# Performance work log

Hardware: AMD Instinct MI355X
Metric: run time of the kernel (lower is better)

The kernel has to match this reference:

```python
import jax, jax.numpy as jnp
import numpy as np

N_NODES = 10000
N_EDGES = 80000
LATENT = 128
OUT_SIZE = 3
NODE_F = 12
EDGE_F = 7
STEPS = 15
LN_EPS = 1e-5


def _mlp(x, W0, b0, W1, b1, W2, b2):
    h = jax.nn.relu(x @ W0 + b0)
    h = jax.nn.relu(h @ W1 + b1)
    return h @ W2 + b2


def _ln(x, g, b):
    m = jnp.mean(x, axis=-1, keepdims=True)
    v = jnp.mean(jnp.square(x - m), axis=-1, keepdims=True)
    return (x - m) * jax.lax.rsqrt(v + LN_EPS) * g + b


def _forward(node_features, edge_features, senders, receivers,
             enW0, enb0, enW1, enb1, enW2, enb2, eng, enbe,
             eeW0, eeb0, eeW1, eeb1, eeW2, eeb2, eeg, eebe,
             beW0, beb0, beW1, beb1, beW2, beb2, beg, bebe,
             bnW0, bnb0, bnW1, bnb1, bnW2, bnb2, bng, bnbe,
             dW0, db0, dW1, db1, dW2, db2):
    # Encoder: node and mesh-edge MLPs with LayerNorm
    nl = _ln(_mlp(node_features, enW0, enb0, enW1, enb1, enW2, enb2), eng, enbe)  # [N, L]
    el = _ln(_mlp(edge_features, eeW0, eeb0, eeW1, eeb1, eeW2, eeb2), eeg, eebe)  # [E, L]

    # Processor: 15 GraphNetBlocks with residual connections, scanned over stacked params
    def block(carry, p):
        n, e = carry
        (eW0, eb0, eW1, eb1, eW2, eb2, eg, ebe,
         nW0, nb0, nW1, nb1, nW2, nb2, ng, nbe) = p
        feat = jnp.concatenate([n[senders], n[receivers], e], axis=-1)  # [E, 3L]
        new_e = _ln(_mlp(feat, eW0, eb0, eW1, eb1, eW2, eb2), eg, ebe)  # [E, L]
        agg = jax.ops.segment_sum(new_e, receivers, num_segments=N_NODES)  # [N, L]
        new_n = _ln(_mlp(jnp.concatenate([n, agg], axis=-1), nW0, nb0, nW1, nb1, nW2, nb2), ng, nbe)
        return (n + new_n, e + new_e), None

    xs = (beW0, beb0, beW1, beb1, beW2, beb2, beg, bebe,
          bnW0, bnb0, bnW1, bnb1, bnW2, bnb2, bng, bnbe)
    (nl, el), _ = jax.lax.scan(jax.checkpoint(block), (nl, el), xs)

    # Decoder: MLP without LayerNorm
    return _mlp(nl, dW0, db0, dW1, db1, dW2, db2)  # [N, OUT_SIZE]


def setup_inputs() -> dict:
    ks = iter(jax.random.split(jax.random.key(0), 32))

    def W(*shape):
        return jax.random.normal(next(ks), shape, jnp.float32) * (1.0 / np.sqrt(shape[-2]))

    z = lambda *s: jnp.zeros(s, jnp.float32)
    o = lambda *s: jnp.ones(s, jnp.float32)
    d = {}
    d['node_features'] = jax.random.normal(next(ks), (N_NODES, NODE_F), jnp.float32)
    d['edge_features'] = jax.random.normal(next(ks), (N_EDGES, EDGE_F), jnp.float32)
    d['senders'] = jax.random.randint(next(ks), (N_EDGES,), 0, N_NODES, jnp.int32)
    d['receivers'] = jax.random.randint(next(ks), (N_EDGES,), 0, N_NODES, jnp.int32)
    d.update(enW0=W(NODE_F, LATENT), enb0=z(LATENT), enW1=W(LATENT, LATENT), enb1=z(LATENT),
             enW2=W(LATENT, LATENT), enb2=z(LATENT), eng=o(LATENT), enbe=z(LATENT))
    d.update(eeW0=W(EDGE_F, LATENT), eeb0=z(LATENT), eeW1=W(LATENT, LATENT), eeb1=z(LATENT),
             eeW2=W(LATENT, LATENT), eeb2=z(LATENT), eeg=o(LATENT), eebe=z(LATENT))
    d.update(beW0=W(STEPS, 3 * LATENT, LATENT), beb0=z(STEPS, LATENT),
             beW1=W(STEPS, LATENT, LATENT), beb1=z(STEPS, LATENT),
             beW2=W(STEPS, LATENT, LATENT), beb2=z(STEPS, LATENT),
             beg=o(STEPS, LATENT), bebe=z(STEPS, LATENT))
    d.update(bnW0=W(STEPS, 2 * LATENT, LATENT), bnb0=z(STEPS, LATENT),
             bnW1=W(STEPS, LATENT, LATENT), bnb1=z(STEPS, LATENT),
             bnW2=W(STEPS, LATENT, LATENT), bnb2=z(STEPS, LATENT),
             bng=o(STEPS, LATENT), bnbe=z(STEPS, LATENT))
    d.update(dW0=W(LATENT, LATENT), db0=z(LATENT), dW1=W(LATENT, LATENT), db1=z(LATENT),
             dW2=W(LATENT, OUT_SIZE), db2=z(OUT_SIZE))
    return d


def reference(node_features, edge_features, senders, receivers,
              enW0, enb0, enW1, enb1, enW2, enb2, eng, enbe,
              eeW0, eeb0, eeW1, eeb1, eeW2, eeb2, eeg, eebe,
              beW0, beb0, beW1, beb1, beW2, beb2, beg, bebe,
              bnW0, bnb0, bnW1, bnb1, bnW2, bnb2, bng, bnbe,
              dW0, db0, dW1, db1, dW2, db2):
    return _forward(node_features, edge_features, senders, receivers,
                    enW0, enb0, enW1, enb1, enW2, enb2, eng, enbe,
                    eeW0, eeb0, eeW1, eeb1, eeW2, eeb2, eeg, eebe,
                    beW0, beb0, beW1, beb1, beW2, beb2, beg, bebe,
                    bnW0, bnb0, bnW1, bnb1, bnW2, bnb2, bng, bnbe,
                    dW0, db0, dW1, db1, dW2, db2)
```

## Files before the change

### kernel.cpp

```cpp
#include <hip/hip_runtime.h>
#include <hip/hip_bf16.h>
#include <stdint.h>

#define N_NODES 10000
#define N_EDGES 80000
#define L 128
#define STEPS 15
#define LN_EPS 1e-5f
#define NTHR 256
#define H_STRIDE 272

typedef short short8 __attribute__((ext_vector_type(8)));
typedef float floatx4 __attribute__((ext_vector_type(4)));

__device__ __forceinline__ float bf2f(const __hip_bfloat16 x) {
    return __bfloat162float(x);
}
__device__ __forceinline__ float ldmix(const void* p, int idx, int isf32) {
    return isf32 ? ((const float*)p)[idx]
                 : bf2f(((const __hip_bfloat16*)p)[idx]);
}

__global__ void detect_dtype(const uint32_t* __restrict__ nf, int* cnt) {
    int c = 0;
    for (int i = blockIdx.x * blockDim.x + threadIdx.x; i < 60000;
         i += gridDim.x * blockDim.x) {
        const uint32_t w = nf[i];
        c += (((w >> 7) & 0xFF) >= 0xC6) + (((w >> 23) & 0xFF) >= 0xC6);
    }
    atomicAdd(cnt, c);
}

#define N_TMATS 14
struct TAll {
    const void* src[N_TMATS];
    long long cum[N_TMATS + 1];
    int K[N_TMATS], N[N_TMATS], Kpad[N_TMATS];
};

__global__ void transpose_all(TAll a, const int* __restrict__ cnt,
                              __hip_bfloat16* __restrict__ pool) {
    const int isf32 = (*cnt > 1000);
    const long long total = a.cum[N_TMATS];
    for (long long i = blockIdx.x * (long long)blockDim.x + threadIdx.x;
         i < total; i += gridDim.x * (long long)blockDim.x) {
        int e = 0;
        #pragma unroll 1
        for (int j = 1; j < N_TMATS; j++) if (i >= a.cum[j]) e = j;
        const long long r = i - a.cum[e];
        const int per = a.N[e] * a.Kpad[e];
        const int m = (int)(r / per);
        const int r2 = (int)(r - (long long)m * per);
        const int nn = r2 / a.Kpad[e];
        const int kk = r2 - nn * a.Kpad[e];
        float v = 0.f;
        if (kk < a.K[e]) v = ldmix(a.src[e], (m * a.K[e] + kk) * a.N[e] + nn, isf32);
        pool[i] = __float2bfloat16(v);
    }
}

__global__ void convert_feats(const void* __restrict__ nf,
                              const void* __restrict__ ef,
                              const int* __restrict__ cnt,
                              const int* __restrict__ elist,
                              __hip_bfloat16* __restrict__ fN,
                              __hip_bfloat16* __restrict__ fE)
{
    const int isf32 = (*cnt > 1000);
    const int totN = N_NODES * 32;
    const int totE = N_EDGES * 32;
    for (int i = blockIdx.x * blockDim.x + threadIdx.x; i < totN + totE;
         i += gridDim.x * blockDim.x) {
        if (i < totN) {
            const int r = i >> 5, c = i & 31;
            fN[i] = __float2bfloat16(c < 12 ? ldmix(nf, r * 12 + c, isf32) : 0.f);
        } else {
            const int j = i - totN;
            const int r = j >> 5, c = j & 31;
            const int e = elist[r];
            fE[j] = __float2bfloat16(c < 7 ? ldmix(ef, e * 7 + c, isf32) : 0.f);
        }
    }
}

__global__ void csr_hist(const int* __restrict__ rcv, int* __restrict__ deg) {
    for (int i = blockIdx.x * blockDim.x + threadIdx.x; i < N_EDGES;
         i += gridDim.x * blockDim.x)
        atomicAdd(&deg[rcv[i]], 1);
}

__global__ void csr_scan(const int* __restrict__ deg, int* __restrict__ rowptr,
                         int* __restrict__ cursor) {
    __shared__ int part[256];
    __shared__ int partx[257];
    const int t = threadIdx.x;
    int s = 0;
    for (int j = 0; j < 40; j++) {
        const int i = t * 40 + j;
        if (i < N_NODES) s += deg[i];
    }
    part[t] = s;
    __syncthreads();
    if (t == 0) {
        int r = 0;
        for (int k = 0; k < 256; k++) { partx[k] = r; r += part[k]; }
        partx[256] = r;
    }
    __syncthreads();
    int run = partx[t];
    for (int j = 0; j < 40; j++) {
        const int i = t * 40 + j;
        if (i < N_NODES) {
            rowptr[i] = run;
            cursor[i] = run;
            run += deg[i];
        }
    }
    if (t == 255) rowptr[N_NODES] = partx[256];
}

__global__ void csr_scatter(const int* __restrict__ rcv, int* __restrict__ cursor,
                            int* __restrict__ elist) {
    for (int i = blockIdx.x * blockDim.x + threadIdx.x; i < N_EDGES;
         i += gridDim.x * blockDim.x) {
        const int p = atomicAdd(&cursor[rcv[i]], 1);
        elist[p] = i;
    }
}

__global__ void sort_meta(const int* __restrict__ snd, const int* __restrict__ rcv,
                          const int* __restrict__ elist,
                          int* __restrict__ ssnd, int* __restrict__ srcv) {
    for (int i = blockIdx.x * blockDim.x + threadIdx.x; i < N_EDGES;
         i += gridDim.x * blockDim.x) {
        const int e = elist[i];
        ssnd[i] = snd[e];
        srcv[i] = rcv[e];
    }
}

__global__ __launch_bounds__(256)
void csr_agg(const int* __restrict__ rowptr,
             const __hip_bfloat16* __restrict__ ln16,
             __hip_bfloat16* __restrict__ agg16)
{
    const int g = threadIdx.x >> 5;
    const int lane = threadIdx.x & 31;
    const int v = blockIdx.x * 8 + g;
    if (v >= N_NODES) return;
    const int c0 = lane * 4;
    float s0 = 0.f, s1 = 0.f, s2 = 0.f, s3 = 0.f;
    int j = rowptr[v];
    const int en = rowptr[v + 1];
    for (; j + 1 < en; j += 2) {
        union { uint2 w; __hip_bfloat16 h[4]; } u0, u1;
        u0.w = *(const uint2*)(ln16 + (size_t)j * L + c0);
        u1.w = *(const uint2*)(ln16 + (size_t)(j + 1) * L + c0);
        s0 += bf2f(u0.h[0]); s1 += bf2f(u0.h[1]); s2 += bf2f(u0.h[2]); s3 += bf2f(u0.h[3]);
        s0 += bf2f(u1.h[0]); s1 += bf2f(u1.h[1]); s2 += bf2f(u1.h[2]); s3 += bf2f(u1.h[3]);
    }
    for (; j < en; j++) {
        union { uint2 w; __hip_bfloat16 h[4]; } u;
        u.w = *(const uint2*)(ln16 + (size_t)j * L + c0);
        s0 += bf2f(u.h[0]); s1 += bf2f(u.h[1]); s2 += bf2f(u.h[2]); s3 += bf2f(u.h[3]);
    }
    union { uint2 w; __hip_bfloat16 h[4]; } o;
    o.h[0] = __float2bfloat16(s0); o.h[1] = __float2bfloat16(s1);
    o.h[2] = __float2bfloat16(s2); o.h[3] = __float2bfloat16(s3);
    *(uint2*)(agg16 + (size_t)v * L + c0) = o.w;
}

enum AMode { A_PLAIN = 0, A_FEAT = 1, A_CAT = 2 };
enum Epi   { E_LN_STORE = 0, E_LN_EDGE = 1, E_LN_NODE = 2, E_DEC = 3 };

template <int AMODE, int EPI, int NL>
__global__ __launch_bounds__(NTHR, 4)
void fused_mlp(const __hip_bfloat16* __restrict__ A, int lda, int M, int K0,
               const __hip_bfloat16* __restrict__ WT0,
               const __hip_bfloat16* __restrict__ WT1,
               const __hip_bfloat16* __restrict__ WT2,
               const void* __restrict__ b0,
               const void* __restrict__ b1,
               const void* __restrict__ b2,
               const void* __restrict__ g,
               const void* __restrict__ beta,
               int poff,
               const int* __restrict__ cnt,
               const __hip_bfloat16* __restrict__ n16,
               const __hip_bfloat16* __restrict__ e16s,
               const __hip_bfloat16* __restrict__ agg16,
               const int* __restrict__ ssnd,
               const int* __restrict__ srcv,
               float* res32,
               __hip_bfloat16* res16,
               __hip_bfloat16* __restrict__ lnout,
               const void* __restrict__ dW,
               const void* __restrict__ db,
               void* __restrict__ dout)
{
    __shared__ __align__(16) char lds[17408 + 10240];
    char* AsB = lds;
    char* WsB = lds + 17408;

    const int nb  = gridDim.x;
    const int per = nb >> 3;
    const int bid = blockIdx.x;
    int sb = bid;
    if (bid < per * 8) sb = (bid & 7) * per + (bid >> 3);

    const int tid  = threadIdx.x;
    const int wv   = tid >> 6;
    const int lane = tid & 63;
    const int quad = lane >> 4;
    const int m15  = lane & 15;
    const int row0 = sb * 64;
    const int isf32 = (*cnt > 1000);

    char* hw = lds + wv * 4352;

    const int boff = m15 * 80 + quad * 16;
    const int aoff = (wv * 16 + m15) * 80 + quad * 16;

    const int aq   = tid & 3;
    const int arow = tid >> 2;
    int sidx = 0, ridx = 0;
    {
        const int rg = row0 + arow;
        if constexpr (AMODE == A_FEAT) {
            sidx = (rg < M) ? ssnd[rg] : 0;
            ridx = (rg < M) ? srcv[rg] : 0;
        }
    }

    auto loadA = [&](int k0) -> int4 {
        const int rg = row0 + arow;
        int4 av = make_int4(0, 0, 0, 0);
        if (rg < M) {
            if constexpr (AMODE == A_PLAIN) {
                av = *(const int4*)(A + (size_t)rg * lda + k0 + aq * 8);
            } else if constexpr (AMODE == A_FEAT) {
                const __hip_bfloat16* sp;
                if (k0 < 2 * L) {
                    const int nd = (k0 < L) ? sidx : ridx;
                    sp = n16 + (size_t)nd * L + (k0 & (L - 1)) + aq * 8;
                } else {
                    sp = e16s + (size_t)rg * L + (k0 - 2 * L) + aq * 8;
                }
                av = *(const int4*)sp;
            } else {
                const __hip_bfloat16* sp = (k0 < L)
                    ? n16   + (size_t)rg * L + k0 + aq * 8
                    : agg16 + (size_t)rg * L + (k0 - L) + aq * 8;
                av = *(const int4*)sp;
            }
        }
        return av;
    };
    auto loadW = [&](const __hip_bfloat16* WT, int ksz, int k0) -> int4 {
        return *(const int4*)(WT + (size_t)(tid >> 2) * ksz + k0 + aq * 8);
    };
    auto loadW2 = [&](const __hip_bfloat16* WT, int ksz, int k0) -> int4 {
        return *(const int4*)(WT + (size_t)((tid >> 2) + 64) * ksz + k0 + aq * 8);
    };

    floatx4 acc[8];

    #pragma unroll
    for (int ct = 0; ct < 8; ct++) acc[ct] = (floatx4)0.f;

    int4 pA = loadA(0);
    int4 pW0 = loadW(WT0, K0, 0);
    int4 pW1 = loadW2(WT0, K0, 0);

    for (int k0 = 0; k0 < K0; k0 += 32) {
        *(int4*)(AsB + arow * 80 + aq * 16) = pA;
        *(int4*)(WsB + arow * 80 + aq * 16)        = pW0;
        *(int4*)(WsB + (arow + 64) * 80 + aq * 16) = pW1;
        __syncthreads();
        if (k0 + 32 < K0) {
            pA  = loadA(k0 + 32);
            pW0 = loadW(WT0, K0, k0 + 32);
            pW1 = loadW2(WT0, K0, k0 + 32);
        }
        const short8 a = *(const short8*)(AsB + aoff);
        #pragma unroll
        for (int ct = 0; ct < 8; ct++) {
            const short8 b = *(const short8*)(WsB + boff + ct * 1280);
            acc[ct] = __builtin_amdgcn_mfma_f32_16x16x32_bf16(a, b, acc[ct], 0, 0, 0);
        }
        __syncthreads();
    }
    {
        float bb[8];
        #pragma unroll
        for (int ct = 0; ct < 8; ct++) bb[ct] = ldmix(b0, poff + ct * 16 + m15, isf32);
        #pragma unroll
        for (int ct = 0; ct < 8; ct++)
            #pragma unroll
            for (int i = 0; i < 4; i++) {
                const int rl = quad * 4 + i;
                const int col = ct * 16 + m15;
                *(__hip_bfloat16*)(hw + rl * H_STRIDE + col * 2) =
                    __float2bfloat16(fmaxf(acc[ct][i] + bb[ct], 0.f));
            }
    }

    {
        #pragma unroll
        for (int ct = 0; ct < 8; ct++) acc[ct] = (floatx4)0.f;
        short8 af[4];
        #pragma unroll
        for (int c = 0; c < 4; c++)
            af[c] = *(const short8*)(hw + m15 * H_STRIDE + c * 64 + quad * 16);
        int4 qW0 = loadW(WT1, L, 0);
        int4 qW1 = loadW2(WT1, L, 0);
        for (int c = 0; c < 4; c++) {
            *(int4*)(WsB + arow * 80 + aq * 16)        = qW0;
            *(int4*)(WsB + (arow + 64) * 80 + aq * 16) = qW1;
            __syncthreads();
            if (c < 3) {
                qW0 = loadW(WT1, L, (c + 1) * 32);
                qW1 = loadW2(WT1, L, (c + 1) * 32);
            }
            #pragma unroll
            for (int ct = 0; ct < 8; ct++) {
                const short8 b = *(const short8*)(WsB + boff + ct * 1280);
                acc[ct] = __builtin_amdgcn_mfma_f32_16x16x32_bf16(af[c], b, acc[ct], 0, 0, 0);
            }
            __syncthreads();
        }
        float bb[8];
        #pragma unroll
        for (int ct = 0; ct < 8; ct++) bb[ct] = ldmix(b1, poff + ct * 16 + m15, isf32);
        #pragma unroll
        for (int ct = 0; ct < 8; ct++)
            #pragma unroll
            for (int i = 0; i < 4; i++) {
                const int rl = quad * 4 + i;
                const int col = ct * 16 + m15;
                *(__hip_bfloat16*)(hw + rl * H_STRIDE + col * 2) =
                    __float2bfloat16(fmaxf(acc[ct][i] + bb[ct], 0.f));
            }
    }

    if constexpr (NL == 3) {
        #pragma unroll
        for (int ct = 0; ct < 8; ct++) acc[ct] = (floatx4)0.f;
        short8 af[4];
        #pragma unroll
        for (int c = 0; c < 4; c++)
            af[c] = *(const short8*)(hw + m15 * H_STRIDE + c * 64 + quad * 16);
        int4 qW0 = loadW(WT2, L, 0);
        int4 qW1 = loadW2(WT2, L, 0);
        for (int c = 0; c < 4; c++) {
            *(int4*)(WsB + arow * 80 + aq * 16)        = qW0;
            *(int4*)(WsB + (arow + 64) * 80 + aq * 16) = qW1;
            __syncthreads();
            if (c < 3) {
                qW0 = loadW(WT2, L, (c + 1) * 32);
                qW1 = loadW2(WT2, L, (c + 1) * 32);
            }
            #pragma unroll
            for (int ct = 0; ct < 8; ct++) {
                const short8 b = *(const short8*)(WsB + boff + ct * 1280);
                acc[ct] = __builtin_amdgcn_mfma_f32_16x16x32_bf16(af[c], b, acc[ct], 0, 0, 0);
            }
            __syncthreads();
        }
        float bb[8], gg[8], be[8];
        #pragma unroll
        for (int ct = 0; ct < 8; ct++) {
            bb[ct] = ldmix(b2,   poff + ct * 16 + m15, isf32);
            gg[ct] = ldmix(g,    poff + ct * 16 + m15, isf32);
            be[ct] = ldmix(beta, poff + ct * 16 + m15, isf32);
        }
        float ov[4][8];
        #pragma unroll
        for (int i = 0; i < 4; i++) {
            float t[8], s = 0.f, s2 = 0.f;
            #pragma unroll
            for (int ct = 0; ct < 8; ct++) {
                t[ct] = acc[ct][i] + bb[ct];
                s  += t[ct];
                s2 += t[ct] * t[ct];
            }
            #pragma unroll
            for (int m = 1; m < 16; m <<= 1) {
                s  += __shfl_xor(s,  m, 64);
                s2 += __shfl_xor(s2, m, 64);
            }
            const float mean = s * (1.f / 128.f);
            const float var  = s2 * (1.f / 128.f) - mean * mean;
            const float inv  = rsqrtf(fmaxf(var, 0.f) + LN_EPS);
            #pragma unroll
            for (int ct = 0; ct < 8; ct++)
                ov[i][ct] = (t[ct] - mean) * inv * gg[ct] + be[ct];
        }
        float* stg = (float*)lds;
        const int mypass = wv >> 1;
        const int rloc   = (wv & 1) * 16 + quad * 4;
        #pragma unroll
        for (int p = 0; p < 2; p++) {
            if (mypass == p) {
                #pragma unroll
                for (int i = 0; i < 4; i++)
                    #pragma unroll
                    for (int ct = 0; ct < 8; ct++)
                        stg[(rloc + i) * 132 + ct * 16 + m15] = ov[i][ct];
            }
            __syncthreads();
            #pragma unroll
            for (int it = 0; it < 4; it++) {
                const int flat = it * NTHR + tid;
                const int r  = flat >> 5;
                const int c4 = (flat & 31) * 4;
                const int rg = row0 + p * 32 + r;
                if (rg < M) {
                    const float4 o4 = *(const float4*)&stg[r * 132 + c4];
                    const size_t idx = (size_t)rg * L + c4;
                    union { uint2 w; __hip_bfloat16 h[4]; } pk;
                    if constexpr (EPI == E_LN_STORE) {
                        *(float4*)&res32[idx] = o4;
                        pk.h[0] = __float2bfloat16(o4.x); pk.h[1] = __float2bfloat16(o4.y);
                        pk.h[2] = __float2bfloat16(o4.z); pk.h[3] = __float2bfloat16(o4.w);
                        *(uint2*)(res16 + idx) = pk.w;
                    } else {
                        float4 nw = *(const float4*)&res32[idx];
                        nw.x += o4.x; nw.y += o4.y; nw.z += o4.z; nw.w += o4.w;
                        *(float4*)&res32[idx] = nw;
                        pk.h[0] = __float2bfloat16(nw.x); pk.h[1] = __float2bfloat16(nw.y);
                        pk.h[2] = __float2bfloat16(nw.z); pk.h[3] = __float2bfloat16(nw.w);
                        *(uint2*)(res16 + idx) = pk.w;
                        if constexpr (EPI == E_LN_EDGE) {
                            pk.h[0] = __float2bfloat16(o4.x); pk.h[1] = __float2bfloat16(o4.y);
                            pk.h[2] = __float2bfloat16(o4.z); pk.h[3] = __float2bfloat16(o4.w);
                            *(uint2*)(lnout + idx) = pk.w;
                        }
                    }
                }
            }
            __syncthreads();
        }
    } else {
        __syncthreads();
        float* Wl = (float*)WsB;
        for (int i = tid; i < 3 * L; i += NTHR) {
            const int o = i / L, k = i - o * L;
            Wl[o * L + k] = ldmix(dW, k * 3 + o, isf32);
        }
        __syncthreads();
        if (tid < 64) {
            const int rg = row0 + tid;
            if (rg < M) {
                const __hip_bfloat16* hr =
                    (const __hip_bfloat16*)(lds + (tid >> 4) * 4352 + (tid & 15) * H_STRIDE);
                float s0 = ldmix(db, 0, isf32);
                float s1 = ldmix(db, 1, isf32);
                float s2 = ldmix(db, 2, isf32);
                #pragma unroll 8
                for (int k = 0; k < L; k++) {
                    const float hv = bf2f(hr[k]);
                    s0 += hv * Wl[k];
                    s1 += hv * Wl[L + k];
                    s2 += hv * Wl[2 * L + k];
                }
                if (isf32) {
                    float* o = (float*)dout;
                    o[rg * 3 + 0] = s0; o[rg * 3 + 1] = s1; o[rg * 3 + 2] = s2;
                } else {
                    __hip_bfloat16* o = (__hip_bfloat16*)dout;
                    o[rg * 3 + 0] = __float2bfloat16(s0);
                    o[rg * 3 + 1] = __float2bfloat16(s1);
                    o[rg * 3 + 2] = __float2bfloat16(s2);
                }
            }
        }
    }
}

extern "C" void kernel_launch(void* const* d_in, const int* in_sizes, int n_in,
                              void* d_out, int out_size, void* d_ws, size_t ws_size,
                              hipStream_t stream)
{
    (void)in_sizes; (void)n_in; (void)out_size; (void)ws_size;
    const int* snd = (const int*)d_in[2];
    const int* rcv = (const int*)d_in[3];

    char* ws = (char*)d_ws;
    int* cnt = (int*)ws;                              ws += 256;
    auto takeB = [&](size_t el) {
        __hip_bfloat16* p = (__hip_bfloat16*)ws;
        ws += ((el * 2 + 255) & ~255ull);
        return p;
    };
    auto takeF = [&](size_t el) {
        float* p = (float*)ws;
        ws += ((el * 4 + 255) & ~255ull);
        return p;
    };
    auto takeI = [&](size_t el) {
        int* p = (int*)ws;
        ws += ((el * 4 + 255) & ~255ull);
        return p;
    };

    const int srcIdx[N_TMATS] = {4, 6, 8, 12, 14, 16, 20, 22, 24, 28, 30, 32, 36, 38};
    const int tK[N_TMATS]    = {12, 128, 128, 7, 128, 128, 384, 128, 128, 256, 128, 128, 128, 128};
    const int tKp[N_TMATS]   = {32, 128, 128, 32, 128, 128, 384, 128, 128, 256, 128, 128, 128, 128};
    const int tNm[N_TMATS]   = {1, 1, 1, 1, 1, 1, STEPS, STEPS, STEPS, STEPS, STEPS, STEPS, 1, 1};
    TAll ta;
    long long cum = 0;
    __hip_bfloat16* wmat[N_TMATS];
    __hip_bfloat16* wpool = (__hip_bfloat16*)ws;
    for (int j = 0; j < N_TMATS; j++) {
        ta.src[j] = d_in[srcIdx[j]];
        ta.cum[j] = cum;
        ta.K[j] = tK[j]; ta.N[j] = 128; ta.Kpad[j] = tKp[j];
        wmat[j] = wpool + cum;
        cum += (long long)tNm[j] * 128 * tKp[j];
    }
    ta.cum[N_TMATS] = cum;
    ws += ((cum * 2 + 255) & ~255ull);

    float* n32 = takeF((size_t)N_NODES * L);
    float* e32 = takeF((size_t)N_EDGES * L);
    __hip_bfloat16* n16   = takeB((size_t)N_NODES * L);
    __hip_bfloat16* e16   = takeB((size_t)N_EDGES * L);
    __hip_bfloat16* ln16  = takeB((size_t)N_EDGES * L);
    __hip_bfloat16* agg16 = takeB((size_t)N_NODES * L);
    __hip_bfloat16* fN16  = takeB((size_t)N_NODES * 32);
    __hip_bfloat16* fE16  = takeB((size_t)N_EDGES * 32);
    int* deg    = takeI(N_NODES);
    int* rowptr = takeI(N_NODES + 1);
    int* cursor = takeI(N_NODES);
    int* elist  = takeI(N_EDGES);
    int* ssnd   = takeI(N_EDGES);
    int* srcv   = takeI(N_EDGES);

    const dim3 blk(NTHR);
    const dim3 grdE((N_EDGES + 63) / 64);
    const dim3 grdN((N_NODES + 63) / 64);

    (void)hipMemsetAsync(cnt, 0, sizeof(int), stream);
    (void)hipMemsetAsync(deg, 0, N_NODES * sizeof(int), stream);
    detect_dtype<<<dim3(64), blk, 0, stream>>>((const uint32_t*)d_in[0], cnt);
    transpose_all<<<dim3(512), blk, 0, stream>>>(ta, cnt, wpool);

    csr_hist<<<dim3(80), blk, 0, stream>>>(rcv, deg);
    csr_scan<<<dim3(1), blk, 0, stream>>>(deg, rowptr, cursor);
    csr_scatter<<<dim3(80), blk, 0, stream>>>(rcv, cursor, elist);
    sort_meta<<<dim3(80), blk, 0, stream>>>(snd, rcv, elist, ssnd, srcv);
    convert_feats<<<dim3(256), blk, 0, stream>>>(d_in[0], d_in[1], cnt, elist, fN16, fE16);

    fused_mlp<A_PLAIN, E_LN_STORE, 3><<<grdE, blk, 0, stream>>>(
        fE16, 32, N_EDGES, 32, wmat[3], wmat[4], wmat[5],
        d_in[13], d_in[15], d_in[17], d_in[18], d_in[19], 0, cnt,
        nullptr, nullptr, nullptr, nullptr, nullptr,
        e32, e16, nullptr, nullptr, nullptr, nullptr);
    fused_mlp<A_PLAIN, E_LN_STORE, 3><<<grdN, blk, 0, stream>>>(
        fN16, 32, N_NODES, 32, wmat[0], wmat[1], wmat[2],
        d_in[5], d_in[7], d_in[9], d_in[10], d_in[11], 0, cnt,
        nullptr, nullptr, nullptr, nullptr, nullptr,
        n32, n16, nullptr, nullptr, nullptr, nullptr);

    for (int s = 0; s < STEPS; s++) {
        const int po = s * L;
        fused_mlp<A_FEAT, E_LN_EDGE, 3><<<grdE, blk, 0, stream>>>(
            nullptr, 0, N_EDGES, 384,
            wmat[6] + (size_t)s * 128 * 384,
            wmat[7] + (size_t)s * 128 * 128,
            wmat[8] + (size_t)s * 128 * 128,
            d_in[21], d_in[23], d_in[25], d_in[26], d_in[27], po, cnt,
            n16, e16, nullptr, ssnd, srcv,
            e32, e16, ln16, nullptr, nullptr, nullptr);
        csr_agg<<<dim3((N_NODES + 7) / 8), blk, 0, stream>>>(rowptr, ln16, agg16);
        fused_mlp<A_CAT, E_LN_NODE, 3><<<grdN, blk, 0, stream>>>(
            nullptr, 0, N_NODES, 256,
            wmat[9]  + (size_t)s * 128 * 256,
            wmat[10] + (size_t)s * 128 * 128,
            wmat[11] + (size_t)s * 128 * 128,
            d_in[29], d_in[31], d_in[33], d_in[34], d_in[35], po, cnt,
            n16, nullptr, agg16, nullptr, nullptr,
            n32, n16, nullptr, nullptr, nullptr, nullptr);
    }

    fused_mlp<A_PLAIN, E_DEC, 2><<<grdN, blk, 0, stream>>>(
        n16, 128, N_NODES, 128, wmat[12], wmat[13], nullptr,
        d_in[37], d_in[39], nullptr, nullptr, nullptr, 0, cnt,
        nullptr, nullptr, nullptr, nullptr, nullptr,
        nullptr, nullptr, nullptr, d_in[40], d_in[41], d_out);
}
```

Baseline: 1.202 ms.

## Fuse segment-sum into edge MLP epilogue with run-length fp32 atomics

Removes the separate CSR aggregation kernel and the bf16 per-edge LN output buffer. The edge MLP epilogue now walks receiver-sorted rows in LDS, sums runs of equal receivers, and does fp32 atomicAdd into an fp32 agg buffer. The node MLP reads agg32, converts it to bf16 on load, and zeroes its rows after use for the next step. This saves a kernel launch and the round trip of the edge-sized buffer, at the cost of atomic traffic and nondeterministic summation order.

```diff
diff --git a/kernel.cpp b/kernel.cpp
--- a/kernel.cpp
+++ b/kernel.cpp
@@ -139,37 +139,6 @@
     }
 }
 
-__global__ __launch_bounds__(256)
-void csr_agg(const int* __restrict__ rowptr,
-             const __hip_bfloat16* __restrict__ ln16,
-             __hip_bfloat16* __restrict__ agg16)
-{
-    const int g = threadIdx.x >> 5;
-    const int lane = threadIdx.x & 31;
-    const int v = blockIdx.x * 8 + g;
-    if (v >= N_NODES) return;
-    const int c0 = lane * 4;
-    float s0 = 0.f, s1 = 0.f, s2 = 0.f, s3 = 0.f;
-    int j = rowptr[v];
-    const int en = rowptr[v + 1];
-    for (; j + 1 < en; j += 2) {
-        union { uint2 w; __hip_bfloat16 h[4]; } u0, u1;
-        u0.w = *(const uint2*)(ln16 + (size_t)j * L + c0);
-        u1.w = *(const uint2*)(ln16 + (size_t)(j + 1) * L + c0);
-        s0 += bf2f(u0.h[0]); s1 += bf2f(u0.h[1]); s2 += bf2f(u0.h[2]); s3 += bf2f(u0.h[3]);
-        s0 += bf2f(u1.h[0]); s1 += bf2f(u1.h[1]); s2 += bf2f(u1.h[2]); s3 += bf2f(u1.h[3]);
-    }
-    for (; j < en; j++) {
-        union { uint2 w; __hip_bfloat16 h[4]; } u;
-        u.w = *(const uint2*)(ln16 + (size_t)j * L + c0);
-        s0 += bf2f(u.h[0]); s1 += bf2f(u.h[1]); s2 += bf2f(u.h[2]); s3 += bf2f(u.h[3]);
-    }
-    union { uint2 w; __hip_bfloat16 h[4]; } o;
-    o.h[0] = __float2bfloat16(s0); o.h[1] = __float2bfloat16(s1);
-    o.h[2] = __float2bfloat16(s2); o.h[3] = __float2bfloat16(s3);
-    *(uint2*)(agg16 + (size_t)v * L + c0) = o.w;
-}
-
 enum AMode { A_PLAIN = 0, A_FEAT = 1, A_CAT = 2 };
 enum Epi   { E_LN_STORE = 0, E_LN_EDGE = 1, E_LN_NODE = 2, E_DEC = 3 };
 
@@ -188,12 +157,11 @@
                const int* __restrict__ cnt,
                const __hip_bfloat16* __restrict__ n16,
                const __hip_bfloat16* __restrict__ e16s,
-               const __hip_bfloat16* __restrict__ agg16,
+               float* __restrict__ agg32,
                const int* __restrict__ ssnd,
                const int* __restrict__ srcv,
                float* res32,
                __hip_bfloat16* res16,
-               __hip_bfloat16* __restrict__ lnout,
                const void* __restrict__ dW,
                const void* __restrict__ db,
                void* __restrict__ dout)
@@ -248,10 +216,19 @@
                 }
                 av = *(const int4*)sp;
             } else {
-                const __hip_bfloat16* sp = (k0 < L)
-                    ? n16   + (size_t)rg * L + k0 + aq * 8
-                    : agg16 + (size_t)rg * L + (k0 - L) + aq * 8;
-                av = *(const int4*)sp;
+                if (k0 < L) {
+                    av = *(const int4*)(n16 + (size_t)rg * L + k0 + aq * 8);
+                } else {
+                    const float* sp = agg32 + (size_t)rg * L + (k0 - L) + aq * 8;
+                    const float4 f0 = *(const float4*)sp;
+                    const float4 f1 = *(const float4*)(sp + 4);
+                    union { int4 v; __hip_bfloat16 h[8]; } u;
+                    u.h[0] = __float2bfloat16(f0.x); u.h[1] = __float2bfloat16(f0.y);
+                    u.h[2] = __float2bfloat16(f0.z); u.h[3] = __float2bfloat16(f0.w);
+                    u.h[4] = __float2bfloat16(f1.x); u.h[5] = __float2bfloat16(f1.y);
+                    u.h[6] = __float2bfloat16(f1.z); u.h[7] = __float2bfloat16(f1.w);
+                    av = u.v;
+                }
             }
         }
         return av;
@@ -397,6 +374,10 @@
                 ov[i][ct] = (t[ct] - mean) * inv * gg[ct] + be[ct];
         }
         float* stg = (float*)lds;
+        int*   sv  = (int*)(lds + 16896);
+        if constexpr (EPI == E_LN_EDGE) {
+            if (tid < 64) sv[tid] = srcv[row0 + tid];
+        }
         const int mypass = wv >> 1;
         const int rloc   = (wv & 1) * 16 + quad * 4;
         #pragma unroll
@@ -431,15 +412,41 @@
                         pk.h[0] = __float2bfloat16(nw.x); pk.h[1] = __float2bfloat16(nw.y);
                         pk.h[2] = __float2bfloat16(nw.z); pk.h[3] = __float2bfloat16(nw.w);
                         *(uint2*)(res16 + idx) = pk.w;
-                        if constexpr (EPI == E_LN_EDGE) {
-                            pk.h[0] = __float2bfloat16(o4.x); pk.h[1] = __float2bfloat16(o4.y);
-                            pk.h[2] = __float2bfloat16(o4.z); pk.h[3] = __float2bfloat16(o4.w);
-                            *(uint2*)(lnout + idx) = pk.w;
-                        }
                     }
                 }
             }
+            if constexpr (EPI == E_LN_EDGE) {
+                const int c = tid & 127;
+                const int h = tid >> 7;
+                const int rbase = p * 32 + h * 16;
+                int vcur = sv[rbase];
+                float a = stg[(h * 16) * 132 + c];
+                #pragma unroll
+                for (int i = 1; i < 16; i++) {
+                    const int v = sv[rbase + i];
+                    const float x = stg[(h * 16 + i) * 132 + c];
+                    if (v != vcur) {
+                        atomicAdd(&agg32[(size_t)vcur * L + c], a);
+                        vcur = v;
+                        a = x;
+                    } else {
+                        a += x;
+                    }
+                }
+                atomicAdd(&agg32[(size_t)vcur * L + c], a);
+            }
             __syncthreads();
+        }
+        if constexpr (AMODE == A_CAT) {
+            #pragma unroll
+            for (int it = 0; it < 8; it++) {
+                const int flat = it * NTHR + tid;
+                const int r  = flat >> 5;
+                const int c4 = (flat & 31) * 4;
+                const int rg = row0 + r;
+                if (rg < M)
+                    *(float4*)&agg32[(size_t)rg * L + c4] = make_float4(0.f, 0.f, 0.f, 0.f);
+            }
         }
     } else {
         __syncthreads();
@@ -522,12 +529,11 @@
     ta.cum[N_TMATS] = cum;
     ws += ((cum * 2 + 255) & ~255ull);
 
-    float* n32 = takeF((size_t)N_NODES * L);
-    float* e32 = takeF((size_t)N_EDGES * L);
+    float* n32   = takeF((size_t)N_NODES * L);
+    float* e32   = takeF((size_t)N_EDGES * L);
+    float* agg32 = takeF((size_t)N_NODES * L);
     __hip_bfloat16* n16   = takeB((size_t)N_NODES * L);
     __hip_bfloat16* e16   = takeB((size_t)N_EDGES * L);
-    __hip_bfloat16* ln16  = takeB((size_t)N_EDGES * L);
-    __hip_bfloat16* agg16 = takeB((size_t)N_NODES * L);
     __hip_bfloat16* fN16  = takeB((size_t)N_NODES * 32);
     __hip_bfloat16* fE16  = takeB((size_t)N_EDGES * 32);
     int* deg    = takeI(N_NODES);
@@ -543,6 +549,7 @@
 
     (void)hipMemsetAsync(cnt, 0, sizeof(int), stream);
     (void)hipMemsetAsync(deg, 0, N_NODES * sizeof(int), stream);
+    (void)hipMemsetAsync(agg32, 0, (size_t)N_NODES * L * sizeof(float), stream);
     detect_dtype<<<dim3(64), blk, 0, stream>>>((const uint32_t*)d_in[0], cnt);
     transpose_all<<<dim3(512), blk, 0, stream>>>(ta, cnt, wpool);
 
@@ -556,12 +563,12 @@
         fE16, 32, N_EDGES, 32, wmat[3], wmat[4], wmat[5],
         d_in[13], d_in[15], d_in[17], d_in[18], d_in[19], 0, cnt,
         nullptr, nullptr, nullptr, nullptr, nullptr,
-        e32, e16, nullptr, nullptr, nullptr, nullptr);
+        e32, e16, nullptr, nullptr, nullptr);
     fused_mlp<A_PLAIN, E_LN_STORE, 3><<<grdN, blk, 0, stream>>>(
         fN16, 32, N_NODES, 32, wmat[0], wmat[1], wmat[2],
         d_in[5], d_in[7], d_in[9], d_in[10], d_in[11], 0, cnt,
         nullptr, nullptr, nullptr, nullptr, nullptr,
-        n32, n16, nullptr, nullptr, nullptr, nullptr);
+        n32, n16, nullptr, nullptr, nullptr);
 
     for (int s = 0; s < STEPS; s++) {
         const int po = s * L;
@@ -571,22 +578,21 @@
             wmat[7] + (size_t)s * 128 * 128,
             wmat[8] + (size_t)s * 128 * 128,
             d_in[21], d_in[23], d_in[25], d_in[26], d_in[27], po, cnt,
-            n16, e16, nullptr, ssnd, srcv,
-            e32, e16, ln16, nullptr, nullptr, nullptr);
-        csr_agg<<<dim3((N_NODES + 7) / 8), blk, 0, stream>>>(rowptr, ln16, agg16);
+            n16, e16, agg32, ssnd, srcv,
+            e32, e16, nullptr, nullptr, nullptr);
         fused_mlp<A_CAT, E_LN_NODE, 3><<<grdN, blk, 0, stream>>>(
             nullptr, 0, N_NODES, 256,
             wmat[9]  + (size_t)s * 128 * 256,
             wmat[10] + (size_t)s * 128 * 128,
             wmat[11] + (size_t)s * 128 * 128,
             d_in[29], d_in[31], d_in[33], d_in[34], d_in[35], po, cnt,
-            n16, nullptr, agg16, nullptr, nullptr,
-            n32, n16, nullptr, nullptr, nullptr, nullptr);
+            n16, nullptr, agg32, nullptr, nullptr,
+            n32, n16, nullptr, nullptr, nullptr);
     }
 
     fused_mlp<A_PLAIN, E_DEC, 2><<<grdN, blk, 0, stream>>>(
         n16, 128, N_NODES, 128, wmat[12], wmat[13], nullptr,
         d_in[37], d_in[39], nullptr, nullptr, nullptr, 0, cnt,
         nullptr, nullptr, nullptr, nullptr, nullptr,
-        nullptr, nullptr, nullptr, d_in[40], d_in[41], d_out);
-}
+        nullptr, nullptr, d_in[40], d_in[41], d_out);
+}
```

Result: slower. 1.232 ms (+2.5%).

## Fuse CSR segment-sum aggregation into node MLP kernel via LDS staging

Applied to the files above, without the earlier changes.

Removes the separate csr_agg kernel and the agg16 global buffer. The node MLP kernel now gathers and sums each node's incoming edge rows from ln16 via rowptr into a 16 KB LDS tile, then reads the second half of its concatenated input from LDS. This saves one launch per step and a global write and read of the aggregate. In exchange the node kernel uses more LDS and its launch-bounds occupancy hint drops to 2, and only 157 blocks do the gather, which may expose latency on the irregular loop.

```diff
diff --git a/kernel.cpp b/kernel.cpp
--- a/kernel.cpp
+++ b/kernel.cpp
@@ -139,42 +139,11 @@
     }
 }
 
-__global__ __launch_bounds__(256)
-void csr_agg(const int* __restrict__ rowptr,
-             const __hip_bfloat16* __restrict__ ln16,
-             __hip_bfloat16* __restrict__ agg16)
-{
-    const int g = threadIdx.x >> 5;
-    const int lane = threadIdx.x & 31;
-    const int v = blockIdx.x * 8 + g;
-    if (v >= N_NODES) return;
-    const int c0 = lane * 4;
-    float s0 = 0.f, s1 = 0.f, s2 = 0.f, s3 = 0.f;
-    int j = rowptr[v];
-    const int en = rowptr[v + 1];
-    for (; j + 1 < en; j += 2) {
-        union { uint2 w; __hip_bfloat16 h[4]; } u0, u1;
-        u0.w = *(const uint2*)(ln16 + (size_t)j * L + c0);
-        u1.w = *(const uint2*)(ln16 + (size_t)(j + 1) * L + c0);
-        s0 += bf2f(u0.h[0]); s1 += bf2f(u0.h[1]); s2 += bf2f(u0.h[2]); s3 += bf2f(u0.h[3]);
-        s0 += bf2f(u1.h[0]); s1 += bf2f(u1.h[1]); s2 += bf2f(u1.h[2]); s3 += bf2f(u1.h[3]);
-    }
-    for (; j < en; j++) {
-        union { uint2 w; __hip_bfloat16 h[4]; } u;
-        u.w = *(const uint2*)(ln16 + (size_t)j * L + c0);
-        s0 += bf2f(u.h[0]); s1 += bf2f(u.h[1]); s2 += bf2f(u.h[2]); s3 += bf2f(u.h[3]);
-    }
-    union { uint2 w; __hip_bfloat16 h[4]; } o;
-    o.h[0] = __float2bfloat16(s0); o.h[1] = __float2bfloat16(s1);
-    o.h[2] = __float2bfloat16(s2); o.h[3] = __float2bfloat16(s3);
-    *(uint2*)(agg16 + (size_t)v * L + c0) = o.w;
-}
-
 enum AMode { A_PLAIN = 0, A_FEAT = 1, A_CAT = 2 };
 enum Epi   { E_LN_STORE = 0, E_LN_EDGE = 1, E_LN_NODE = 2, E_DEC = 3 };
 
-template <int AMODE, int EPI, int NL>
-__global__ __launch_bounds__(NTHR, 4)
+template <int AMODE, int EPI, int NL, int MINW>
+__global__ __launch_bounds__(NTHR, MINW)
 void fused_mlp(const __hip_bfloat16* __restrict__ A, int lda, int M, int K0,
                const __hip_bfloat16* __restrict__ WT0,
                const __hip_bfloat16* __restrict__ WT1,
@@ -188,7 +157,8 @@
                const int* __restrict__ cnt,
                const __hip_bfloat16* __restrict__ n16,
                const __hip_bfloat16* __restrict__ e16s,
-               const __hip_bfloat16* __restrict__ agg16,
+               const __hip_bfloat16* __restrict__ lnsrc,
+               const int* __restrict__ rowptr,
                const int* __restrict__ ssnd,
                const int* __restrict__ srcv,
                float* res32,
@@ -198,7 +168,8 @@
                const void* __restrict__ db,
                void* __restrict__ dout)
 {
-    __shared__ __align__(16) char lds[17408 + 10240];
+    constexpr int LDSB = 27648 + ((AMODE == A_CAT) ? 16384 : 0);
+    __shared__ __align__(16) char lds[LDSB];
     char* AsB = lds;
     char* WsB = lds + 17408;
 
@@ -220,6 +191,33 @@
 
     const int boff = m15 * 80 + quad * 16;
     const int aoff = (wv * 16 + m15) * 80 + quad * 16;
+
+    if constexpr (AMODE == A_CAT) {
+        __hip_bfloat16* AgL = (__hip_bfloat16*)(lds + 27648);
+        #pragma unroll
+        for (int it = 0; it < 4; it++) {
+            const int item = it * NTHR + tid;
+            const int nl = item >> 4;
+            const int ch = item & 15;
+            const int rg = row0 + nl;
+            float s[8] = {0.f, 0.f, 0.f, 0.f, 0.f, 0.f, 0.f, 0.f};
+            if (rg < M) {
+                const int jb = rowptr[rg];
+                const int je = rowptr[rg + 1];
+                for (int j = jb; j < je; j++) {
+                    union { int4 v; __hip_bfloat16 h[8]; } u;
+                    u.v = *(const int4*)(lnsrc + (size_t)j * L + ch * 8);
+                    #pragma unroll
+                    for (int q = 0; q < 8; q++) s[q] += bf2f(u.h[q]);
+                }
+            }
+            union { int4 v; __hip_bfloat16 h[8]; } o;
+            #pragma unroll
+            for (int q = 0; q < 8; q++) o.h[q] = __float2bfloat16(s[q]);
+            *(int4*)(AgL + nl * L + ch * 8) = o.v;
+        }
+        __syncthreads();
+    }
 
     const int aq   = tid & 3;
     const int arow = tid >> 2;
@@ -248,10 +246,12 @@
                 }
                 av = *(const int4*)sp;
             } else {
-                const __hip_bfloat16* sp = (k0 < L)
-                    ? n16   + (size_t)rg * L + k0 + aq * 8
-                    : agg16 + (size_t)rg * L + (k0 - L) + aq * 8;
-                av = *(const int4*)sp;
+                if (k0 < L) {
+                    av = *(const int4*)(n16 + (size_t)rg * L + k0 + aq * 8);
+                } else {
+                    const __hip_bfloat16* AgL = (const __hip_bfloat16*)(lds + 27648);
+                    av = *(const int4*)(AgL + arow * L + (k0 - L) + aq * 8);
+                }
             }
         }
         return av;
@@ -527,7 +527,6 @@
     __hip_bfloat16* n16   = takeB((size_t)N_NODES * L);
     __hip_bfloat16* e16   = takeB((size_t)N_EDGES * L);
     __hip_bfloat16* ln16  = takeB((size_t)N_EDGES * L);
-    __hip_bfloat16* agg16 = takeB((size_t)N_NODES * L);
     __hip_bfloat16* fN16  = takeB((size_t)N_NODES * 32);
     __hip_bfloat16* fE16  = takeB((size_t)N_EDGES * 32);
     int* deg    = takeI(N_NODES);
@@ -552,41 +551,40 @@
     sort_meta<<<dim3(80), blk, 0, stream>>>(snd, rcv, elist, ssnd, srcv);
     convert_feats<<<dim3(256), blk, 0, stream>>>(d_in[0], d_in[1], cnt, elist, fN16, fE16);
 
-    fused_mlp<A_PLAIN, E_LN_STORE, 3><<<grdE, blk, 0, stream>>>(
+    fused_mlp<A_PLAIN, E_LN_STORE, 3, 4><<<grdE, blk, 0, stream>>>(
         fE16, 32, N_EDGES, 32, wmat[3], wmat[4], wmat[5],
         d_in[13], d_in[15], d_in[17], d_in[18], d_in[19], 0, cnt,
-        nullptr, nullptr, nullptr, nullptr, nullptr,
+        nullptr, nullptr, nullptr, nullptr, nullptr, nullptr,
         e32, e16, nullptr, nullptr, nullptr, nullptr);
-    fused_mlp<A_PLAIN, E_LN_STORE, 3><<<grdN, blk, 0, stream>>>(
+    fused_mlp<A_PLAIN, E_LN_STORE, 3, 4><<<grdN, blk, 0, stream>>>(
         fN16, 32, N_NODES, 32, wmat[0], wmat[1], wmat[2],
         d_in[5], d_in[7], d_in[9], d_in[10], d_in[11], 0, cnt,
-        nullptr, nullptr, nullptr, nullptr, nullptr,
+        nullptr, nullptr, nullptr, nullptr, nullptr, nullptr,
         n32, n16, nullptr, nullptr, nullptr, nullptr);
 
     for (int s = 0; s < STEPS; s++) {
         const int po = s * L;
-        fused_mlp<A_FEAT, E_LN_EDGE, 3><<<grdE, blk, 0, stream>>>(
+        fused_mlp<A_FEAT, E_LN_EDGE, 3, 4><<<grdE, blk, 0, stream>>>(
             nullptr, 0, N_EDGES, 384,
             wmat[6] + (size_t)s * 128 * 384,
             wmat[7] + (size_t)s * 128 * 128,
             wmat[8] + (size_t)s * 128 * 128,
             d_in[21], d_in[23], d_in[25], d_in[26], d_in[27], po, cnt,
-            n16, e16, nullptr, ssnd, srcv,
+            n16, e16, nullptr, nullptr, ssnd, srcv,
             e32, e16, ln16, nullptr, nullptr, nullptr);
-        csr_agg<<<dim3((N_NODES + 7) / 8), blk, 0, stream>>>(rowptr, ln16, agg16);
-        fused_mlp<A_CAT, E_LN_NODE, 3><<<grdN, blk, 0, stream>>>(
+        fused_mlp<A_CAT, E_LN_NODE, 3, 2><<<grdN, blk, 0, stream>>>(
             nullptr, 0, N_NODES, 256,
             wmat[9]  + (size_t)s * 128 * 256,
             wmat[10] + (size_t)s * 128 * 128,
             wmat[11] + (size_t)s * 128 * 128,
             d_in[29], d_in[31], d_in[33], d_in[34], d_in[35], po, cnt,
-            n16, nullptr, agg16, nullptr, nullptr,
+            n16, nullptr, ln16, rowptr, nullptr, nullptr,
             n32, n16, nullptr, nullptr, nullptr, nullptr);
     }
 
-    fused_mlp<A_PLAIN, E_DEC, 2><<<grdN, blk, 0, stream>>>(
+    fused_mlp<A_PLAIN, E_DEC, 2, 4><<<grdN, blk, 0, stream>>>(
         n16, 128, N_NODES, 128, wmat[12], wmat[13], nullptr,
         d_in[37], d_in[39], nullptr, nullptr, nullptr, 0, cnt,
-        nullptr, nullptr, nullptr, nullptr, nullptr,
+        nullptr, nullptr, nullptr, nullptr, nullptr, nullptr,
         nullptr, nullptr, nullptr, d_in[40], d_in[41], d_out);
 }
```

New measurement: 1.394 ms. +16.0%, slower.
